# Performance work log

Hardware: AMD Instinct MI355X
Metric: run time of the kernel (lower is better)

The kernel has to match this reference:

```python
import jax, jax.numpy as jnp
import numpy as np

B, S, E, H = 4, 2048, 1024, 16
D = E // H  # head_dim = 64


def setup_inputs() -> dict:
    key = jax.random.key(0)
    k1, k2, k3 = jax.random.split(key, 3)
    x = jax.random.normal(k1, (B, S, E), dtype=jnp.float32)
    w_attn = jax.random.normal(k2, (E, 3 * E), dtype=jnp.float32) * (E ** -0.5)
    b_attn = jnp.zeros((3 * E,), dtype=jnp.float32)
    w_out = jax.random.normal(k3, (E, E), dtype=jnp.float32) * (E ** -0.5)
    b_out = jnp.zeros((E,), dtype=jnp.float32)
    return {"x": x, "w_attn": w_attn, "b_attn": b_attn, "w_out": w_out, "b_out": b_out}


def reference(x, w_attn, b_attn, w_out, b_out):
    b, s, e = x.shape
    qkv = x @ w_attn + b_attn                      # [b, s, 3e]
    q, k, v = jnp.split(qkv, 3, axis=2)
    q = q.reshape(b, s, H, D)
    k = k.reshape(b, s, H, D)
    v = v.reshape(b, s, H, D)
    energy = jnp.einsum('nqhd,nkhd->nhqk', q, k)   # [b, H, s, s]
    causal = jnp.tril(jnp.ones((s, s), dtype=bool))
    energy = jnp.where(causal, energy, -jnp.inf)
    scale = jnp.sqrt(jnp.float32(D))
    attn = jax.nn.softmax(energy / scale, axis=-1)  # dropout_rate=0.0 -> identity
    out = jnp.einsum('nhql,nlhd->nqhd', attn, v).reshape(b, s, e)
    return out @ w_out + b_out
```

## Files before the change

kernel.cpp:

```cpp
#include <hip/hip_runtime.h>

typedef short bf16x8 __attribute__((ext_vector_type(8)));
typedef float f32x4 __attribute__((ext_vector_type(4)));
typedef float f32x16 __attribute__((ext_vector_type(16)));
typedef float float4v __attribute__((ext_vector_type(4)));
typedef short short4v __attribute__((ext_vector_type(4)));
typedef unsigned uint2v __attribute__((ext_vector_type(2)));
typedef unsigned uint4v __attribute__((ext_vector_type(4)));

#define B_ 4
#define S_ 2048
#define E_ 1024
#define H_ 16
#define D_ 64
#define M_ (B_*S_)
#define N1_ (3*E_)

__device__ inline short f2bs(float f) {
    unsigned u = __builtin_bit_cast(unsigned, f);
    unsigned r = u + 0x7fffu + ((u >> 16) & 1u);
    return (short)(r >> 16);
}
__device__ inline float exp2a(float x) {
    float r; asm("v_exp_f32 %0, %1" : "=v"(r) : "v"(x)); return r;
}
__device__ inline unsigned cvtpk(float a, float b) {
    unsigned r; asm("v_cvt_pk_bf16_f32 %0, %1, %2" : "=v"(r) : "v"(a), "v"(b)); return r;
}

__device__ inline const __attribute__((address_space(1))) void* gas(const void* p) {
    return (const __attribute__((address_space(1))) void*)p;
}
__device__ inline __attribute__((address_space(3))) void* las(void* p) {
    return (__attribute__((address_space(3))) void*)p;
}

__global__ void convert_f32_bf16(const float* __restrict__ in, short* __restrict__ out, int n) {
    int tid = blockIdx.x * blockDim.x + threadIdx.x;
    int stride = gridDim.x * blockDim.x;
    for (int i = tid * 4; i < n; i += stride * 4) {
        float4v v = *(const float4v*)&in[i];
        short4v o;
        o[0] = f2bs(v[0]); o[1] = f2bs(v[1]); o[2] = f2bs(v[2]); o[3] = f2bs(v[3]);
        *(short4v*)&out[i] = o;
    }
}

__global__ void transpose_convert(const float* __restrict__ in, short* __restrict__ out,
                                  int rows, int cols) {
    __shared__ float t[32][33];
    int bx = blockIdx.x * 32;
    int by = blockIdx.y * 32;
    int tx = threadIdx.x, ty = threadIdx.y;
#pragma unroll
    for (int i = 0; i < 4; ++i)
        t[ty + i * 8][tx] = in[(size_t)(by + ty + i * 8) * cols + bx + tx];
    __syncthreads();
#pragma unroll
    for (int i = 0; i < 4; ++i)
        out[(size_t)(bx + ty + i * 8) * rows + by + tx] = f2bs(t[tx][ty + i * 8]);
}

#define MFMA12(Q) \
    _Pragma("unroll") for (int mf = 0; mf < 2; ++mf) \
    _Pragma("unroll") for (int nf = 0; nf < 3; ++nf) { \
        acc[(Q)*2+mf][nf] = __builtin_amdgcn_mfma_f32_16x16x32_bf16(af[mf][0], bfrag[nf][0], acc[(Q)*2+mf][nf], 0, 0, 0); \
        acc[(Q)*2+mf][nf] = __builtin_amdgcn_mfma_f32_16x16x32_bf16(af[mf][1], bfrag[nf][1], acc[(Q)*2+mf][nf], 0, 0, 0); \
    }

#define PHASE(Q, STAGE_STMT, WAITV) do { \
    bf16x8 af[2][2]; \
    _Pragma("unroll") for (int mf = 0; mf < 2; ++mf) \
    _Pragma("unroll") for (int ks = 0; ks < 2; ++ks) { \
        int r = (Q)*32 + mf*16 + li; \
        af[mf][ks] = *(const bf16x8*)(lA + r*128 + ((ks*64 + g*16) ^ ((r & 7) << 4))); \
    } \
    STAGE_STMT; \
    __builtin_amdgcn_s_barrier(); \
    asm volatile("s_waitcnt lgkmcnt(0)" ::: "memory"); \
    __builtin_amdgcn_sched_barrier(0); \
    __builtin_amdgcn_s_setprio(1); \
    MFMA12(Q); \
    __builtin_amdgcn_s_setprio(0); \
    WAITV; \
    __builtin_amdgcn_s_barrier(); \
} while (0)

#define VMW(n) asm volatile("s_waitcnt vmcnt(" #n ")" ::: "memory")
#define NOP_ ((void)0)

__global__ __launch_bounds__(512, 2) void gemm_qkv(
    const short* __restrict__ A, const short* __restrict__ Bt,
    const float* __restrict__ bias,
    short* __restrict__ Qb, short* __restrict__ Kb, short* __restrict__ Vt) {
    __shared__ __attribute__((aligned(16))) short ldsA[2][16384];
    __shared__ __attribute__((aligned(16))) short ldsB[2][12288];
    const int tid = threadIdx.x;
    const int lane = tid & 63;
    const int wid = tid >> 6;
    const int li = lane & 15, g = lane >> 4;
    const int wr = wid >> 2, wc = wid & 3;
    const int Kdim = E_;
    const int NT = Kdim >> 6;

    const int id = blockIdx.x;
    const int swz = (id & 7) * 64 + (id >> 3);
    const int bx = swz & 15, by = swz >> 4;
    const int row0 = by * 256, col0 = bx * 192;

    const int rstage = wid * 8 + (lane >> 3);
    const int cstage = (((lane & 7) ^ ((lane >> 3) & 7)) << 4);

    auto stageA = [&](int buf, int kt, int seg) {
#pragma unroll
        for (int h = 0; h < 2; ++h) {
            const char* src = (const char*)A +
                ((size_t)(row0 + h * 128 + seg * 64 + rstage) * Kdim + kt * 64) * 2 + cstage;
            char* dst = (char*)&ldsA[buf][0] + (h * 2 + seg) * 8192 + wid * 1024;
            __builtin_amdgcn_global_load_lds(gas(src), las(dst), 16, 0, 0);
        }
    };
    auto stageB = [&](int buf, int kt) {
#pragma unroll
        for (int i = 0; i < 3; ++i) {
            const char* src = (const char*)Bt +
                ((size_t)(col0 + i * 64 + rstage) * Kdim + kt * 64) * 2 + cstage;
            char* dst = (char*)&ldsB[buf][0] + i * 8192 + wid * 1024;
            __builtin_amdgcn_global_load_lds(gas(src), las(dst), 16, 0, 0);
        }
    };

    f32x4 acc[8][3];
#pragma unroll
    for (int m = 0; m < 8; ++m)
#pragma unroll
        for (int n = 0; n < 3; ++n) acc[m][n] = (f32x4){0.f, 0.f, 0.f, 0.f};

    stageB(0, 0);
    stageA(0, 0, 0);
    stageA(0, 0, 1);
    asm volatile("s_waitcnt vmcnt(0)" ::: "memory");
    __syncthreads();

    for (int t = 0; t < NT; ++t) {
        const int cur = t & 1;
        const int nb = cur ^ 1;
        const int tn = t + 1;
        const bool st = (tn < NT);
        const char* lA = (const char*)&ldsA[cur][0] + wr * 16384;
        const char* lB = (const char*)&ldsB[cur][0];

        bf16x8 bfrag[3][2];
#pragma unroll
        for (int nf = 0; nf < 3; ++nf)
#pragma unroll
            for (int ks = 0; ks < 2; ++ks) {
                int r = wc * 48 + nf * 16 + li;
                bfrag[nf][ks] = *(const bf16x8*)(lB + r * 128 + ((ks * 64 + g * 16) ^ ((r & 7) << 4)));
            }
        if (st) {
            PHASE(0, stageB(nb, tn), NOP_);
            PHASE(1, stageA(nb, tn, 0), VMW(5));
            PHASE(2, stageA(nb, tn, 1), NOP_);
            PHASE(3, NOP_, VMW(2));
        } else {
            PHASE(0, NOP_, NOP_);
            PHASE(1, NOP_, VMW(0));
            PHASE(2, NOP_, NOP_);
            PHASE(3, NOP_, NOP_);
        }
    }

#pragma unroll
    for (int nf = 0; nf < 3; ++nf) {
        int ncolg = col0 + wc * 48 + nf * 16 + li;
        float bv = bias[ncolg];
        int part = ncolg >> 10;
        int rem = ncolg & 1023;
        if (part < 2) {
            short* Dst = (part == 0) ? Qb : Kb;
#pragma unroll
            for (int mi = 0; mi < 8; ++mi) {
                int rbase = row0 + wr * 128 + mi * 16 + 4 * g;
#pragma unroll
                for (int j = 0; j < 4; ++j)
                    Dst[(size_t)(rbase + j) * E_ + rem] = f2bs(acc[mi][nf][j] + bv);
            }
        } else {
            int h = rem >> 6, d = rem & 63;
#pragma unroll
            for (int mi = 0; mi < 8; ++mi) {
                int s0 = row0 + wr * 128 + mi * 16 + 4 * g;
                int bb2 = s0 >> 11;
                int ss = s0 & 2047;
                uint2v p;
                p[0] = cvtpk(acc[mi][nf][0] + bv, acc[mi][nf][1] + bv);
                p[1] = cvtpk(acc[mi][nf][2] + bv, acc[mi][nf][3] + bv);
                *(uint2v*)&Vt[((size_t)(bb2 * H_ + h) * D_ + d) * S_ + ss] = p;
            }
        }
    }
}

__global__ __launch_bounds__(256, 2) void gemm_bt_out(
    const short* __restrict__ A, const short* __restrict__ Bt,
    const float* __restrict__ bias, float* __restrict__ Cf,
    int Kdim, int Ndim) {
    __shared__ __attribute__((aligned(16))) short As[128 * 32];
    __shared__ __attribute__((aligned(16))) short Bs[128 * 32];
    const int lane = threadIdx.x & 63;
    const int wv = threadIdx.x >> 6;
    const int row0 = blockIdx.y * 128;
    const int col0 = blockIdx.x * 128;
    const int wr = (wv >> 1) * 64;
    const int wc = (wv & 1) * 64;
    const int li = lane & 15;
    const int g = lane >> 4;
    const int lr = lane >> 2;
    const int lk = (lane & 3) * 8;

    f32x4 acc[4][4];
#pragma unroll
    for (int m = 0; m < 4; ++m)
#pragma unroll
        for (int n = 0; n < 4; ++n) acc[m][n] = (f32x4){0.f, 0.f, 0.f, 0.f};

    for (int k0 = 0; k0 < Kdim; k0 += 32) {
#pragma unroll
        for (int i = 0; i < 2; ++i) {
            int cc = wv * 2 + i;
            const short* ga = A + (size_t)(row0 + cc * 16 + lr) * Kdim + k0 + lk;
            __builtin_amdgcn_global_load_lds(gas(ga), las(&As[cc * 512]), 16, 0, 0);
            const short* gb = Bt + (size_t)(col0 + cc * 16 + lr) * Kdim + k0 + lk;
            __builtin_amdgcn_global_load_lds(gas(gb), las(&Bs[cc * 512]), 16, 0, 0);
        }
        __syncthreads();
        bf16x8 af[4], bfr[4];
#pragma unroll
        for (int m = 0; m < 4; ++m) af[m] = *(const bf16x8*)&As[(wr + 16 * m + li) * 32 + g * 8];
#pragma unroll
        for (int n = 0; n < 4; ++n) bfr[n] = *(const bf16x8*)&Bs[(wc + 16 * n + li) * 32 + g * 8];
#pragma unroll
        for (int m = 0; m < 4; ++m)
#pragma unroll
            for (int n = 0; n < 4; ++n)
                acc[m][n] = __builtin_amdgcn_mfma_f32_16x16x32_bf16(af[m], bfr[n], acc[m][n], 0, 0, 0);
        __syncthreads();
    }

#pragma unroll
    for (int n = 0; n < 4; ++n) {
        int ncol = col0 + wc + 16 * n + li;
        float bv = bias[ncol];
#pragma unroll
        for (int m = 0; m < 4; ++m) {
            int rbase = row0 + wr + 16 * m + 4 * g;
#pragma unroll
            for (int j = 0; j < 4; ++j)
                Cf[(size_t)(rbase + j) * Ndim + ncol] = acc[m][n][j] + bv;
        }
    }
}

__global__ __launch_bounds__(256, 4) void attn_kernel(
    const short* __restrict__ Qb, const short* __restrict__ Kb,
    const short* __restrict__ Vt, short* __restrict__ Ob) {
    __shared__ __attribute__((aligned(16))) short Kl[4096];
    __shared__ __attribute__((aligned(16))) short Vl[4096];
    const int lane = threadIdx.x & 63;
    const int wv = threadIdx.x >> 6;
    const int l31 = lane & 31;
    const int hi = lane >> 5;
    const int id = blockIdx.x;
    const int xcd = id & 7;
    const int r_ = id >> 3;
    const int qt = 15 - (r_ >> 3);
    const int bh = xcd * 8 + (r_ & 7);
    const int bb = bh >> 4, hh = bh & 15;
    const short* Qh = Qb + (size_t)bb * (S_ * E_) + hh * 64;
    const short* Kh = Kb + (size_t)bb * (S_ * E_) + hh * 64;
    const short* Vh = Vt + (size_t)bh * (D_ * S_);
    const float CEXP = 0.18033688011112042f;

    const int rstage = wv * 8 + (lane >> 3);
    const int cstage = (((lane & 7) ^ ((lane >> 3) & 7)) << 4);

    const int q0w = qt * 128 + wv * 32;
    const int q = q0w + l31;

    bf16x8 qf[4];
#pragma unroll
    for (int c = 0; c < 4; ++c)
        qf[c] = *(const bf16x8*)&Qh[(size_t)q * E_ + c * 16 + hi * 8];

    f32x16 acc[2];
#pragma unroll
    for (int d = 0; d < 2; ++d)
#pragma unroll
        for (int r = 0; r < 16; ++r) acc[d][r] = 0.f;
    float m = -3e38f, mC = 0.f, l = 0.f;

    const int nw = (q0w + 95) >> 6;
    const int nt = (qt * 128 + 191) >> 6;

    for (int it = 0; it < nt; ++it) {
        const int kt0 = it * 64;
#pragma unroll
        for (int half = 0; half < 2; ++half) {
            const char* gk = (const char*)(Kh + (size_t)(kt0 + half * 32 + rstage) * E_) + cstage;
            __builtin_amdgcn_global_load_lds(gas(gk), las((char*)Kl + half * 4096 + wv * 1024), 16, 0, 0);
            const char* gv = (const char*)Vh + (size_t)(half * 32 + rstage) * (S_ * 2) + (size_t)kt0 * 2 + cstage;
            __builtin_amdgcn_global_load_lds(gas(gv), las((char*)Vl + half * 4096 + wv * 1024), 16, 0, 0);
        }
        __syncthreads();
        if (it < nw) {
            f32x16 sc0, sc1;
#pragma unroll
            for (int r = 0; r < 16; ++r) { sc0[r] = 0.f; sc1[r] = 0.f; }
#pragma unroll
            for (int c = 0; c < 4; ++c) {
                const int r0 = l31, r1 = 32 + l31;
                bf16x8 kf0 = *(const bf16x8*)((const char*)Kl + r0 * 128 +
                                              ((c * 32 + hi * 16) ^ ((r0 & 7) << 4)));
                bf16x8 kf1 = *(const bf16x8*)((const char*)Kl + r1 * 128 +
                                              ((c * 32 + hi * 16) ^ ((r1 & 7) << 4)));
                sc0 = __builtin_amdgcn_mfma_f32_32x32x16_bf16(kf0, qf[c], sc0, 0, 0, 0);
                sc1 = __builtin_amdgcn_mfma_f32_32x32x16_bf16(kf1, qf[c], sc1, 0, 0, 0);
            }
            if (kt0 + 63 > q0w) {
                const int kb = kt0 + 4 * hi;
#pragma unroll
                for (int r = 0; r < 16; ++r) {
                    int key = kb + (r & 3) + 8 * (r >> 2);
                    sc0[r] = (key > q) ? -3e38f : sc0[r];
                    sc1[r] = (key + 32 > q) ? -3e38f : sc1[r];
                }
            }
            float tmx[8];
#pragma unroll
            for (int r = 0; r < 8; ++r)
                tmx[r] = fmaxf(fmaxf(sc0[2 * r], sc0[2 * r + 1]),
                               fmaxf(sc1[2 * r], sc1[2 * r + 1]));
            float tm = fmaxf(fmaxf(fmaxf(tmx[0], tmx[1]), fmaxf(tmx[2], tmx[3])),
                             fmaxf(fmaxf(tmx[4], tmx[5]), fmaxf(tmx[6], tmx[7])));
            tm = fmaxf(tm, __shfl_xor(tm, 32, 64));
            bool need = (tm > m + 16.0f);
            if (__ballot((int)need) != 0ull) {
                float mn = fmaxf(m, tm);
                float sf = exp2a((m - mn) * CEXP);
                m = mn; mC = mn * CEXP;
                l *= sf;
#pragma unroll
                for (int d = 0; d < 2; ++d)
#pragma unroll
                    for (int r = 0; r < 16; ++r) acc[d][r] *= sf;
            }
#pragma unroll
            for (int r = 0; r < 16; ++r) {
                sc0[r] = exp2a(fmaf(sc0[r], CEXP, -mC));
                sc1[r] = exp2a(fmaf(sc1[r], CEXP, -mC));
            }
            float s0 = 0.f, s1 = 0.f;
#pragma unroll
            for (int r = 0; r < 8; ++r) {
                s0 += sc0[2 * r] + sc0[2 * r + 1];
                s1 += sc1[2 * r] + sc1[2 * r + 1];
            }
            float ls = s0 + s1;
            ls += __shfl_xor(ls, 32, 64);
            l += ls;
            const bool lo = (hi == 0);
            bf16x8 pf[4];
#pragma unroll
            for (int s = 0; s < 2; ++s) {
                const f32x16& p = s ? sc1 : sc0;
                unsigned W0 = cvtpk(p[0], p[1]),   W1 = cvtpk(p[2], p[3]);
                unsigned W2 = cvtpk(p[4], p[5]),   W3 = cvtpk(p[6], p[7]);
                unsigned W4 = cvtpk(p[8], p[9]),   W5 = cvtpk(p[10], p[11]);
                unsigned W6 = cvtpk(p[12], p[13]), W7 = cvtpk(p[14], p[15]);
                unsigned xW0 = __shfl_xor(W0, 32, 64), xW1 = __shfl_xor(W1, 32, 64);
                unsigned xW2 = __shfl_xor(W2, 32, 64), xW3 = __shfl_xor(W3, 32, 64);
                unsigned xW4 = __shfl_xor(W4, 32, 64), xW5 = __shfl_xor(W5, 32, 64);
                unsigned xW6 = __shfl_xor(W6, 32, 64), xW7 = __shfl_xor(W7, 32, 64);
                uint4v u1, u2;
                u1[0] = lo ? W0 : xW2;  u1[1] = lo ? W1 : xW3;
                u1[2] = lo ? xW0 : W2;  u1[3] = lo ? xW1 : W3;
                u2[0] = lo ? W4 : xW6;  u2[1] = lo ? W5 : xW7;
                u2[2] = lo ? xW4 : W6;  u2[3] = lo ? xW5 : W7;
                pf[s * 2] = __builtin_bit_cast(bf16x8, u1);
                pf[s * 2 + 1] = __builtin_bit_cast(bf16x8, u2);
            }
#pragma unroll
            for (int db = 0; db < 2; ++db) {
                const int row = db * 32 + l31;
                const int rsw = (row & 7) << 4;
                const char* vrow = (const char*)Vl + row * 128;
                bf16x8 v0 = *(const bf16x8*)(vrow + ((hi * 16) ^ rsw));
                bf16x8 v1 = *(const bf16x8*)(vrow + ((32 + hi * 16) ^ rsw));
                bf16x8 v2 = *(const bf16x8*)(vrow + ((64 + hi * 16) ^ rsw));
                bf16x8 v3 = *(const bf16x8*)(vrow + ((96 + hi * 16) ^ rsw));
                acc[db] = __builtin_amdgcn_mfma_f32_32x32x16_bf16(v0, pf[0], acc[db], 0, 0, 0);
                acc[db] = __builtin_amdgcn_mfma_f32_32x32x16_bf16(v1, pf[1], acc[db], 0, 0, 0);
                acc[db] = __builtin_amdgcn_mfma_f32_32x32x16_bf16(v2, pf[2], acc[db], 0, 0, 0);
                acc[db] = __builtin_amdgcn_mfma_f32_32x32x16_bf16(v3, pf[3], acc[db], 0, 0, 0);
            }
        }
        __syncthreads();
    }

    float rl = __builtin_amdgcn_rcpf(l);
    short* orow = Ob + ((size_t)(bb * S_ + q)) * E_ + hh * 64;
#pragma unroll
    for (int db = 0; db < 2; ++db)
#pragma unroll
        for (int rb = 0; rb < 4; ++rb) {
            uint2v pk;
            pk[0] = cvtpk(acc[db][rb * 4 + 0] * rl, acc[db][rb * 4 + 1] * rl);
            pk[1] = cvtpk(acc[db][rb * 4 + 2] * rl, acc[db][rb * 4 + 3] * rl);
            *(uint2v*)&orow[db * 32 + rb * 8 + hi * 4] = pk;
        }
}

extern "C" void kernel_launch(void* const* d_in, const int* in_sizes, int n_in,
                              void* d_out, int out_size, void* d_ws, size_t ws_size,
                              hipStream_t stream) {
    const float* x      = (const float*)d_in[0];
    const float* w_attn = (const float*)d_in[1];
    const float* b_attn = (const float*)d_in[2];
    const float* w_out  = (const float*)d_in[3];
    const float* b_out  = (const float*)d_in[4];
    float* out = (float*)d_out;

    char* ws = (char*)d_ws;
    short* Xbf  = (short*)(ws);
    short* Wat  = (short*)(ws + (16ull << 20));
    short* Wot  = (short*)(ws + (22ull << 20));
    short* Qb   = (short*)(ws + (24ull << 20));
    short* Kb   = (short*)(ws + (40ull << 20));
    short* Vt   = (short*)(ws + (56ull << 20));
    short* Obuf = Xbf;

    convert_f32_bf16<<<2048, 256, 0, stream>>>(x, Xbf, M_ * E_);
    transpose_convert<<<dim3(N1_ / 32, E_ / 32), dim3(32, 8), 0, stream>>>(w_attn, Wat, E_, N1_);
    transpose_convert<<<dim3(E_ / 32, E_ / 32), dim3(32, 8), 0, stream>>>(w_out, Wot, E_, E_);

    gemm_qkv<<<512, 512, 0, stream>>>(Xbf, Wat, b_attn, Qb, Kb, Vt);

    attn_kernel<<<1024, 256, 0, stream>>>(Qb, Kb, Vt, Obuf);

    gemm_bt_out<<<dim3(E_ / 128, M_ / 128), 256, 0, stream>>>(
        Obuf, Wot, b_out, out, E_, E_);
}
```

Measured before the change: 176.6 us.

## Replace output GEMM with 8-wave double-buffered pipelined kernel; front-load QKV staging

The simple output-projection GEMM, which used a 128x128 tile, 32-wide K steps and a full sync every step, is replaced. The new kernel uses 512 threads, a 256x128 tile, 64-wide K steps, swizzled LDS, double-buffered global-to-LDS loads with phased MFMA scheduling, setprio, and an XCD-aware block remap. This is meant to hide load latency and raise MFMA utilisation in the final GEMM. Separately, the QKV GEMM now issues all next-tile stage loads in phase 0 and adjusts its vmcnt waits, which changes how loads overlap with compute. The larger tile gives only 256 blocks, which may leave some CUs underused.

After: 175.6 us. About the same (-0.6%).

```diff
diff --git a/kernel.cpp b/kernel.cpp
--- a/kernel.cpp
+++ b/kernel.cpp
@@ -159,9 +159,9 @@
                 bfrag[nf][ks] = *(const bf16x8*)(lB + r * 128 + ((ks * 64 + g * 16) ^ ((r & 7) << 4)));
             }
         if (st) {
-            PHASE(0, stageB(nb, tn), NOP_);
-            PHASE(1, stageA(nb, tn, 0), VMW(5));
-            PHASE(2, stageA(nb, tn, 1), NOP_);
+            PHASE(0, { stageB(nb, tn); stageA(nb, tn, 0); stageA(nb, tn, 1); }, NOP_);
+            PHASE(1, NOP_, VMW(7));
+            PHASE(2, NOP_, NOP_);
             PHASE(3, NOP_, VMW(2));
         } else {
             PHASE(0, NOP_, NOP_);
@@ -202,62 +202,122 @@
     }
 }
 
-__global__ __launch_bounds__(256, 2) void gemm_bt_out(
+#define MFMA8(Q) \
+    _Pragma("unroll") for (int mf = 0; mf < 2; ++mf) \
+    _Pragma("unroll") for (int nf = 0; nf < 2; ++nf) { \
+        acc[(Q)*2+mf][nf] = __builtin_amdgcn_mfma_f32_16x16x32_bf16(af[mf][0], bfrag[nf][0], acc[(Q)*2+mf][nf], 0, 0, 0); \
+        acc[(Q)*2+mf][nf] = __builtin_amdgcn_mfma_f32_16x16x32_bf16(af[mf][1], bfrag[nf][1], acc[(Q)*2+mf][nf], 0, 0, 0); \
+    }
+
+#define PHASE8(Q, STAGE_STMT, WAITV) do { \
+    bf16x8 af[2][2]; \
+    _Pragma("unroll") for (int mf = 0; mf < 2; ++mf) \
+    _Pragma("unroll") for (int ks = 0; ks < 2; ++ks) { \
+        int r = (Q)*32 + mf*16 + li; \
+        af[mf][ks] = *(const bf16x8*)(lA + r*128 + ((ks*64 + g*16) ^ ((r & 7) << 4))); \
+    } \
+    STAGE_STMT; \
+    __builtin_amdgcn_s_barrier(); \
+    asm volatile("s_waitcnt lgkmcnt(0)" ::: "memory"); \
+    __builtin_amdgcn_sched_barrier(0); \
+    __builtin_amdgcn_s_setprio(1); \
+    MFMA8(Q); \
+    __builtin_amdgcn_s_setprio(0); \
+    WAITV; \
+    __builtin_amdgcn_s_barrier(); \
+} while (0)
+
+__global__ __launch_bounds__(512, 2) void gemm_out8(
     const short* __restrict__ A, const short* __restrict__ Bt,
-    const float* __restrict__ bias, float* __restrict__ Cf,
-    int Kdim, int Ndim) {
-    __shared__ __attribute__((aligned(16))) short As[128 * 32];
-    __shared__ __attribute__((aligned(16))) short Bs[128 * 32];
-    const int lane = threadIdx.x & 63;
-    const int wv = threadIdx.x >> 6;
-    const int row0 = blockIdx.y * 128;
-    const int col0 = blockIdx.x * 128;
-    const int wr = (wv >> 1) * 64;
-    const int wc = (wv & 1) * 64;
-    const int li = lane & 15;
-    const int g = lane >> 4;
-    const int lr = lane >> 2;
-    const int lk = (lane & 3) * 8;
-
-    f32x4 acc[4][4];
-#pragma unroll
-    for (int m = 0; m < 4; ++m)
-#pragma unroll
-        for (int n = 0; n < 4; ++n) acc[m][n] = (f32x4){0.f, 0.f, 0.f, 0.f};
-
-    for (int k0 = 0; k0 < Kdim; k0 += 32) {
+    const float* __restrict__ bias, float* __restrict__ Cf) {
+    __shared__ __attribute__((aligned(16))) short ldsA[2][2][2][4096];
+    __shared__ __attribute__((aligned(16))) short ldsB[2][8192];
+    const int tid = threadIdx.x;
+    const int lane = tid & 63;
+    const int wid = tid >> 6;
+    const int li = lane & 15, g = lane >> 4;
+    const int wr = wid >> 2, wc = wid & 3;
+    const int Kdim = E_;
+    const int NT = Kdim >> 6;
+
+    const int id = blockIdx.x;
+    const int swz = (id & 7) * 32 + (id >> 3);
+    const int bx = swz & 7, by = swz >> 3;
+    const int row0 = by * 256, col0 = bx * 128;
+
+    const int rstage = wid * 8 + (lane >> 3);
+    const int cstage = (((lane & 7) ^ ((lane >> 3) & 7)) << 4);
+
+    auto stageA = [&](int buf, int kt, int seg) {
+#pragma unroll
+        for (int h = 0; h < 2; ++h) {
+            const char* src = (const char*)A +
+                ((size_t)(row0 + h * 128 + seg * 64 + rstage) * Kdim + kt * 64) * 2 + cstage;
+            char* dst = (char*)&ldsA[buf][h][seg][0] + wid * 1024;
+            __builtin_amdgcn_global_load_lds(gas(src), las(dst), 16, 0, 0);
+        }
+    };
+    auto stageB = [&](int buf, int kt) {
 #pragma unroll
         for (int i = 0; i < 2; ++i) {
-            int cc = wv * 2 + i;
-            const short* ga = A + (size_t)(row0 + cc * 16 + lr) * Kdim + k0 + lk;
-            __builtin_amdgcn_global_load_lds(gas(ga), las(&As[cc * 512]), 16, 0, 0);
-            const short* gb = Bt + (size_t)(col0 + cc * 16 + lr) * Kdim + k0 + lk;
-            __builtin_amdgcn_global_load_lds(gas(gb), las(&Bs[cc * 512]), 16, 0, 0);
-        }
-        __syncthreads();
-        bf16x8 af[4], bfr[4];
-#pragma unroll
-        for (int m = 0; m < 4; ++m) af[m] = *(const bf16x8*)&As[(wr + 16 * m + li) * 32 + g * 8];
-#pragma unroll
-        for (int n = 0; n < 4; ++n) bfr[n] = *(const bf16x8*)&Bs[(wc + 16 * n + li) * 32 + g * 8];
-#pragma unroll
-        for (int m = 0; m < 4; ++m)
-#pragma unroll
-            for (int n = 0; n < 4; ++n)
-                acc[m][n] = __builtin_amdgcn_mfma_f32_16x16x32_bf16(af[m], bfr[n], acc[m][n], 0, 0, 0);
-        __syncthreads();
-    }
-
-#pragma unroll
-    for (int n = 0; n < 4; ++n) {
-        int ncol = col0 + wc + 16 * n + li;
+            const char* src = (const char*)Bt +
+                ((size_t)(col0 + i * 64 + rstage) * Kdim + kt * 64) * 2 + cstage;
+            char* dst = (char*)&ldsB[buf][0] + i * 8192 + wid * 1024;
+            __builtin_amdgcn_global_load_lds(gas(src), las(dst), 16, 0, 0);
+        }
+    };
+
+    f32x4 acc[8][2];
+#pragma unroll
+    for (int m = 0; m < 8; ++m)
+#pragma unroll
+        for (int n = 0; n < 2; ++n) acc[m][n] = (f32x4){0.f, 0.f, 0.f, 0.f};
+
+    stageB(0, 0);
+    stageA(0, 0, 0);
+    stageA(0, 0, 1);
+    asm volatile("s_waitcnt vmcnt(0)" ::: "memory");
+    __syncthreads();
+
+    for (int t = 0; t < NT; ++t) {
+        const int cur = t & 1;
+        const int nb = cur ^ 1;
+        const int tn = t + 1;
+        const bool st = (tn < NT);
+        const char* lA = (const char*)&ldsA[cur][wr][0][0];
+        const char* lB = (const char*)&ldsB[cur][0];
+
+        bf16x8 bfrag[2][2];
+#pragma unroll
+        for (int nf = 0; nf < 2; ++nf)
+#pragma unroll
+            for (int ks = 0; ks < 2; ++ks) {
+                int r = wc * 32 + nf * 16 + li;
+                bfrag[nf][ks] = *(const bf16x8*)(lB + r * 128 + ((ks * 64 + g * 16) ^ ((r & 7) << 4)));
+            }
+        if (st) {
+            PHASE8(0, stageB(nb, tn), NOP_);
+            PHASE8(1, stageA(nb, tn, 0), VMW(4));
+            PHASE8(2, stageA(nb, tn, 1), NOP_);
+            PHASE8(3, NOP_, VMW(2));
+        } else {
+            PHASE8(0, NOP_, NOP_);
+            PHASE8(1, NOP_, VMW(0));
+            PHASE8(2, NOP_, NOP_);
+            PHASE8(3, NOP_, NOP_);
+        }
+    }
+
+#pragma unroll
+    for (int nf = 0; nf < 2; ++nf) {
+        int ncol = col0 + wc * 32 + nf * 16 + li;
         float bv = bias[ncol];
 #pragma unroll
-        for (int m = 0; m < 4; ++m) {
-            int rbase = row0 + wr + 16 * m + 4 * g;
+        for (int mi = 0; mi < 8; ++mi) {
+            int rbase = row0 + wr * 128 + mi * 16 + 4 * g;
 #pragma unroll
             for (int j = 0; j < 4; ++j)
-                Cf[(size_t)(rbase + j) * Ndim + ncol] = acc[m][n][j] + bv;
+                Cf[(size_t)(rbase + j) * E_ + ncol] = acc[mi][nf][j] + bv;
         }
     }
 }
@@ -448,6 +508,5 @@
 
     attn_kernel<<<1024, 256, 0, stream>>>(Qb, Kb, Vt, Obuf);
 
-    gemm_bt_out<<<dim3(E_ / 128, M_ / 128), 256, 0, stream>>>(
-        Obuf, Wot, b_out, out, E_, E_);
-}
+    gemm_out8<<<256, 512, 0, stream>>>(Obuf, Wot, b_out, out);
+}
```
